# Kernel optimization log

Hardware: AMD Instinct MI355X
Metric: run time of the kernel (lower is better)

The kernel has to match this reference:

```python
import jax, jax.numpy as jnp
import numpy as np

N_FEATURE = 1024
N_HEAD = 16
DK = N_FEATURE // N_HEAD
SCALE = float(np.sqrt(DK))
LN_EPS = 1e-5


def setup_inputs() -> dict:
    key = jax.random.key(0)
    ks = jax.random.split(key, 12)
    B, T, F = 4, 2048, N_FEATURE
    s = 1.0 / np.sqrt(F)
    inp = {
        "key": jax.random.normal(ks[0], (B, T, F), jnp.float32),
        "value": jax.random.normal(ks[1], (B, T, F), jnp.float32),
        "query": jax.random.normal(ks[2], (B, T, F), jnp.float32),
        "Wq": jax.random.uniform(ks[3], (F, F), jnp.float32, -s, s),
        "bq": jax.random.uniform(ks[4], (F,), jnp.float32, -s, s),
        "Wk": jax.random.uniform(ks[5], (F, F), jnp.float32, -s, s),
        "bk": jax.random.uniform(ks[6], (F,), jnp.float32, -s, s),
        "Wv": jax.random.uniform(ks[7], (F, F), jnp.float32, -s, s),
        "bv": jax.random.uniform(ks[8], (F,), jnp.float32, -s, s),
        "Wo": jax.random.uniform(ks[9], (F, F), jnp.float32, -s, s),
        "bo": jax.random.uniform(ks[10], (F,), jnp.float32, -s, s),
        "ln_g": jnp.ones((F,), jnp.float32),
        "ln_b": jnp.zeros((F,), jnp.float32),
    }
    return inp


def reference(key, value, query, Wq, bq, Wk, bk, Wv, bv, Wo, bo, ln_g, ln_b):
    # key/value/query: [B, T, F]. torch chunk(n_head, -1) == reshape to (B,T,H,dk).
    B, T, F = query.shape
    residual = query
    q = (query @ Wq.T + bq).reshape(B, T, N_HEAD, DK)
    k = (key @ Wk.T + bk).reshape(B, T, N_HEAD, DK)
    v = (value @ Wv.T + bv).reshape(B, T, N_HEAD, DK)
    # scores: [B, H, Tq, Tk]
    scores = jnp.einsum("bqhd,bkhd->bhqk", q, k) / SCALE
    attn = jax.nn.softmax(scores, axis=-1)
    ctx = jnp.einsum("bhqk,bkhd->bqhd", attn, v).reshape(B, T, F)
    out = ctx @ Wo.T + bo  # dropout in eval mode = identity
    x = residual + out
    mu = jnp.mean(x, axis=-1, keepdims=True)
    var = jnp.mean(jnp.square(x - mu), axis=-1, keepdims=True)
    return (x - mu) * jax.lax.rsqrt(var + LN_EPS) * ln_g + ln_b
```

## Files before the change

### kernel.cpp

```cpp
#include <hip/hip_runtime.h>
#include <hip/hip_bf16.h>
#include <cstdint>
#include <cstddef>

#define DEVI __device__ __forceinline__

typedef __attribute__((ext_vector_type(8))) short short8;
typedef __attribute__((ext_vector_type(4))) float f32x4;
typedef __attribute__((ext_vector_type(16))) float f32x16;
typedef __attribute__((ext_vector_type(4))) unsigned int u32x4;

constexpr int Bz = 4, Tt = 2048, Fd = 1024, Hh = 16, Dk = 64;
constexpr int Mrows = Bz * Tt;
constexpr float QSCALE = 0.18033688011112042f;

DEVI unsigned short f2bf(float f) {
  union { __hip_bfloat16 h; unsigned short u; } cv;
  cv.h = __float2bfloat16(f);
  return cv.u;
}

DEVI unsigned cvtpk(float a, float b) {
  unsigned r;
  asm("v_cvt_pk_bf16_f32 %0, %1, %2" : "=v"(r) : "v"(a), "v"(b));
  return r;
}

DEVI void gl_lds16(const void* g, void* s) {
  __builtin_amdgcn_global_load_lds(
      (const __attribute__((address_space(1))) void*)g,
      (__attribute__((address_space(3))) void*)s, 16, 0, 0);
}

__global__ void cvt4_bf16(const float* __restrict__ s0, unsigned short* __restrict__ d0,
                          const float* __restrict__ s1, unsigned short* __restrict__ d1,
                          const float* __restrict__ s2, unsigned short* __restrict__ d2,
                          const float* __restrict__ s3, unsigned short* __restrict__ d3,
                          int n4) {
  const float* src = blockIdx.y == 0 ? s0 : (blockIdx.y == 1 ? s1 : (blockIdx.y == 2 ? s2 : s3));
  unsigned short* dst = blockIdx.y == 0 ? d0 : (blockIdx.y == 1 ? d1 : (blockIdx.y == 2 ? d2 : d3));
  int i = blockIdx.x * blockDim.x + threadIdx.x;
  int stride = gridDim.x * blockDim.x;
  for (; i < n4; i += stride) {
    float4 v = reinterpret_cast<const float4*>(src)[i];
    ushort4 o;
    o.x = f2bf(v.x); o.y = f2bf(v.y); o.z = f2bf(v.z); o.w = f2bf(v.w);
    reinterpret_cast<ushort4*>(dst)[i] = o;
  }
}

__global__ __launch_bounds__(256, 2) void gemm_qkvf(
    const float* __restrict__ q32, const float* __restrict__ k32,
    const float* __restrict__ v32, const unsigned short* __restrict__ wq,
    const unsigned short* __restrict__ wk, const unsigned short* __restrict__ wv,
    const float* __restrict__ bq, const float* __restrict__ bk, const float* __restrict__ bv,
    unsigned short* __restrict__ Qb, unsigned short* __restrict__ Kb,
    unsigned short* __restrict__ Vt) {
  constexpr int K = 1024, N = 1024;
  __shared__ __align__(16) unsigned short As[128 * 64];
  __shared__ __align__(16) unsigned short Bs[128 * 64];
  int z = blockIdx.z;
  const float* A32 = z == 0 ? q32 : (z == 1 ? k32 : v32);
  const unsigned short* W = z == 0 ? wq : (z == 1 ? wk : wv);
  const float* bias = z == 0 ? bq : (z == 1 ? bk : bv);
  void* out = z == 0 ? (void*)Qb : (z == 1 ? (void*)Kb : (void*)Vt);
  float scale = z == 0 ? QSCALE : 1.0f;
  int mode = z == 2 ? 2 : 0;

  int f = blockIdx.y * gridDim.x + blockIdx.x;
  f = (f & 7) * 64 + (f >> 3);
  const int m0 = (f >> 3) * 128, n0 = (f & 7) * 128;
  const int t = threadIdx.x, w = t >> 6, l = t & 63;
  const int wr = w >> 1, wc = w & 1;
  const int lr = l & 15, lg = l >> 4;
  f32x4 acc[4][4] = {};

  for (int k0 = 0; k0 < K; k0 += 64) {
    __syncthreads();
    float4 fA[4][2];
#pragma unroll
    for (int i = 0; i < 4; ++i) {
      int row = i * 32 + w * 8 + (l >> 3);
      const float* src = A32 + (size_t)(m0 + row) * K + k0 + (l & 7) * 8;
      fA[i][0] = ((const float4*)src)[0];
      fA[i][1] = ((const float4*)src)[1];
    }
#pragma unroll
    for (int i = 0; i < 4; ++i) {
      int base = i * 4096 + w * 1024;
      int d = base + l * 16;
      int row = d >> 7;
      int srcb = ((l & 7) ^ (row & 7)) << 4;
      gl_lds16((const char*)W + ((size_t)(n0 + row) * K + k0) * 2 + srcb, (char*)Bs + base);
    }
#pragma unroll
    for (int i = 0; i < 4; ++i) {
      int row = i * 32 + w * 8 + (l >> 3);
      u32x4 wv4;
      wv4[0] = cvtpk(fA[i][0].x, fA[i][0].y);
      wv4[1] = cvtpk(fA[i][0].z, fA[i][0].w);
      wv4[2] = cvtpk(fA[i][1].x, fA[i][1].y);
      wv4[3] = cvtpk(fA[i][1].z, fA[i][1].w);
      int slot = (l & 7) ^ (row & 7);
      *(u32x4*)((char*)As + row * 128 + slot * 16) = wv4;
    }
    __syncthreads();
#pragma unroll
    for (int kk = 0; kk < 2; ++kk) {
      short8 af[4], bf[4];
#pragma unroll
      for (int i = 0; i < 4; ++i) {
        int ra = wr * 64 + i * 16 + lr;
        int rb = wc * 64 + i * 16 + lr;
        af[i] = *(const short8*)((const char*)As + ra * 128 + (((kk * 4 + lg) ^ (ra & 7)) << 4));
        bf[i] = *(const short8*)((const char*)Bs + rb * 128 + (((kk * 4 + lg) ^ (rb & 7)) << 4));
      }
#pragma unroll
      for (int mi = 0; mi < 4; ++mi)
#pragma unroll
        for (int ni = 0; ni < 4; ++ni)
          acc[mi][ni] = __builtin_amdgcn_mfma_f32_16x16x32_bf16(af[mi], bf[ni], acc[mi][ni], 0, 0, 0);
    }
  }
#pragma unroll
  for (int mi = 0; mi < 4; ++mi)
#pragma unroll
    for (int ni = 0; ni < 4; ++ni) {
      int col = n0 + wc * 64 + ni * 16 + lr;
      float bv = bias[col];
      if (mode == 2) {
        int hh = col >> 6, dd = col & 63;
        int row = m0 + wr * 64 + mi * 16 + lg * 4;
        int bb = row >> 11, t0 = row & 2047;
        ushort4 o;
        o.x = f2bf(acc[mi][ni][0] + bv);
        o.y = f2bf(acc[mi][ni][1] + bv);
        o.z = f2bf(acc[mi][ni][2] + bv);
        o.w = f2bf(acc[mi][ni][3] + bv);
        *(ushort4*)((unsigned short*)out + (((size_t)(bb * Hh + hh) * Dk + dd) << 11) + t0) = o;
      } else {
#pragma unroll
        for (int r = 0; r < 4; ++r) {
          int row = m0 + wr * 64 + mi * 16 + lg * 4 + r;
          ((unsigned short*)out)[(size_t)row * N + col] = f2bf((acc[mi][ni][r] + bv) * scale);
        }
      }
    }
}

__global__ __launch_bounds__(256, 2) void gemm_out(
    const unsigned short* __restrict__ A, const unsigned short* __restrict__ W,
    const float* __restrict__ bias, const float* __restrict__ resid,
    float* __restrict__ out) {
  constexpr int K = 1024, N = 1024;
  __shared__ __align__(16) unsigned short As[128 * 64];
  __shared__ __align__(16) unsigned short Bs[128 * 64];
  int f = blockIdx.y * gridDim.x + blockIdx.x;
  f = (f & 7) * 64 + (f >> 3);
  const int m0 = (f >> 3) * 128, n0 = (f & 7) * 128;
  const int t = threadIdx.x, w = t >> 6, l = t & 63;
  const int wr = w >> 1, wc = w & 1;
  const int lr = l & 15, lg = l >> 4;
  f32x4 acc[4][4] = {};
  for (int k0 = 0; k0 < K; k0 += 64) {
    __syncthreads();
#pragma unroll
    for (int i = 0; i < 4; ++i) {
      int base = i * 4096 + w * 1024;
      int d = base + l * 16;
      int row = d >> 7;
      int srcb = ((l & 7) ^ (row & 7)) << 4;
      gl_lds16((const char*)A + ((size_t)(m0 + row) * K + k0) * 2 + srcb, (char*)As + base);
      gl_lds16((const char*)W + ((size_t)(n0 + row) * K + k0) * 2 + srcb, (char*)Bs + base);
    }
    __syncthreads();
#pragma unroll
    for (int kk = 0; kk < 2; ++kk) {
      short8 af[4], bf[4];
#pragma unroll
      for (int i = 0; i < 4; ++i) {
        int ra = wr * 64 + i * 16 + lr;
        int rb = wc * 64 + i * 16 + lr;
        af[i] = *(const short8*)((const char*)As + ra * 128 + (((kk * 4 + lg) ^ (ra & 7)) << 4));
        bf[i] = *(const short8*)((const char*)Bs + rb * 128 + (((kk * 4 + lg) ^ (rb & 7)) << 4));
      }
#pragma unroll
      for (int mi = 0; mi < 4; ++mi)
#pragma unroll
        for (int ni = 0; ni < 4; ++ni)
          acc[mi][ni] = __builtin_amdgcn_mfma_f32_16x16x32_bf16(af[mi], bf[ni], acc[mi][ni], 0, 0, 0);
    }
  }
#pragma unroll
  for (int mi = 0; mi < 4; ++mi)
#pragma unroll
    for (int ni = 0; ni < 4; ++ni) {
      int col = n0 + wc * 64 + ni * 16 + lr;
      float bv = bias[col];
#pragma unroll
      for (int r = 0; r < 4; ++r) {
        int row = m0 + wr * 64 + mi * 16 + lg * 4 + r;
        size_t idx = (size_t)row * N + col;
        out[idx] = acc[mi][ni][r] + bv + resid[idx];
      }
    }
}

__global__ __launch_bounds__(512, 2) void attn_kernel(
    const unsigned short* __restrict__ Qb, const unsigned short* __restrict__ Kb,
    const unsigned short* __restrict__ Vt, unsigned short* __restrict__ Ctx) {
  __shared__ __align__(16) unsigned short smem[16 * 4096];
  int bid = blockIdx.x;
  const int xcd = bid & 7, idx = bid >> 3;
  const int bh = xcd * 8 + (idx >> 2);
  const int q0 = (idx & 3) * 512;
  const int h = bh & 15;
  const int b = bh >> 4;
  const int t = threadIdx.x, w = t >> 6, l = t & 63;
  const int q31 = l & 31, hi = l >> 5;
  const int qbase = q0 + w * 64;

  short8 qfA[4], qfB[4];
  {
    const unsigned short* qpA = Qb + (size_t)(b * Tt + qbase + q31) * Fd + h * Dk;
    const unsigned short* qpB = qpA + (size_t)32 * Fd;
#pragma unroll
    for (int c = 0; c < 4; ++c) {
      qfA[c] = *(const short8*)(qpA + c * 16 + hi * 8);
      qfB[c] = *(const short8*)(qpB + c * 16 + hi * 8);
    }
  }

  int koff[8];
#pragma unroll
  for (int g = 0; g < 2; ++g)
#pragma unroll
    for (int c = 0; c < 4; ++c) {
      int row = g * 32 + q31;
      koff[g * 4 + c] = row * 128 + ((c * 32 + hi * 16) ^ ((row & 7) << 4));
    }

  const size_t kbase = (size_t)(b * Tt) * Fd + h * Dk;
  const size_t vbase = (size_t)((b * Hh + h) * Dk) * Tt;

  f32x16 OA0{}, OA1{}, OB0{}, OB1{};
  short8 pfA[4], pfB[4];
  float lsA0 = 0.f, lsB0 = 0.f, lsA1 = 0.f, lsB1 = 0.f;

  auto kbuf = [&](int kt) { return (const char*)smem + ((kt & 7) << 13); };
  auto vbuf = [&](int kt) { return (const char*)smem + 65536 + ((kt & 7) << 13); };

  auto stage = [&](int kt) {
    char* Kd = (char*)smem + ((kt & 7) << 13);
    char* Vd = (char*)smem + 65536 + ((kt & 7) << 13);
    int base = w * 1024;
    int d0 = base + l * 16;
    int row = d0 >> 7, inb = d0 & 127;
    int srcb = inb ^ ((row & 7) << 4);
    gl_lds16((const char*)Kb + (kbase + (size_t)(kt * 64 + row) * Fd) * 2 + srcb, Kd + base);
    gl_lds16((const char*)Vt + (vbase + (size_t)row * Tt + kt * 64) * 2 + srcb, Vd + base);
  };

  auto qk = [&](int kt, f32x16& S0a, f32x16& S1a, f32x16& S0b, f32x16& S1b) {
    const char* Kd = kbuf(kt);
    __builtin_amdgcn_s_setprio(1);
#pragma unroll
    for (int c = 0; c < 4; ++c) {
      short8 k0 = *(const short8*)(Kd + koff[c]);
      short8 k1 = *(const short8*)(Kd + koff[4 + c]);
      S0a = __builtin_amdgcn_mfma_f32_32x32x16_bf16(k0, qfA[c], S0a, 0, 0, 0);
      S1a = __builtin_amdgcn_mfma_f32_32x32x16_bf16(k1, qfA[c], S1a, 0, 0, 0);
      S0b = __builtin_amdgcn_mfma_f32_32x32x16_bf16(k0, qfB[c], S0b, 0, 0, 0);
      S1b = __builtin_amdgcn_mfma_f32_32x32x16_bf16(k1, qfB[c], S1b, 0, 0, 0);
    }
    __builtin_amdgcn_s_setprio(0);
  };

  auto pv = [&](int kt) {
    const char* Vd = vbuf(kt);
    __builtin_amdgcn_s_setprio(1);
#pragma unroll
    for (int db = 0; db < 2; ++db)
#pragma unroll
      for (int kvc = 0; kvc < 4; ++kvc) {
        short8 vf = *(const short8*)(Vd + koff[db * 4 + kvc]);
        if (db == 0) {
          OA0 = __builtin_amdgcn_mfma_f32_32x32x16_bf16(vf, pfA[kvc], OA0, 0, 0, 0);
          OB0 = __builtin_amdgcn_mfma_f32_32x32x16_bf16(vf, pfB[kvc], OB0, 0, 0, 0);
        } else {
          OA1 = __builtin_amdgcn_mfma_f32_32x32x16_bf16(vf, pfA[kvc], OA1, 0, 0, 0);
          OB1 = __builtin_amdgcn_mfma_f32_32x32x16_bf16(vf, pfB[kvc], OB1, 0, 0, 0);
        }
      }
    __builtin_amdgcn_s_setprio(0);
  };

  auto softmax_pack = [&](const f32x16& S0, const f32x16& S1, float& lsA, float& lsB, short8* pf) {
    unsigned pk0[8], pk1[8];
#pragma unroll
    for (int j = 0; j < 8; ++j) {
      int r = j * 2;
      float a0 = __builtin_amdgcn_exp2f(S0[r]);
      float a1 = __builtin_amdgcn_exp2f(S0[r + 1]);
      float b0 = __builtin_amdgcn_exp2f(S1[r]);
      float b1 = __builtin_amdgcn_exp2f(S1[r + 1]);
      lsA += a0 + a1;
      lsB += b0 + b1;
      pk0[j] = cvtpk(a0, a1);
      pk1[j] = cvtpk(b0, b1);
    }
#pragma unroll
    for (int kc = 0; kc < 2; ++kc) {
      unsigned a0 = pk0[kc * 4 + 0], a2 = pk0[kc * 4 + 2];
      unsigned a1 = pk0[kc * 4 + 1], a3 = pk0[kc * 4 + 3];
      asm("v_permlane32_swap_b32 %0, %1" : "+v"(a0), "+v"(a2));
      asm("v_permlane32_swap_b32 %0, %1" : "+v"(a1), "+v"(a3));
      unsigned b0 = pk1[kc * 4 + 0], b2 = pk1[kc * 4 + 2];
      unsigned b1 = pk1[kc * 4 + 1], b3 = pk1[kc * 4 + 3];
      asm("v_permlane32_swap_b32 %0, %1" : "+v"(b0), "+v"(b2));
      asm("v_permlane32_swap_b32 %0, %1" : "+v"(b1), "+v"(b3));
      u32x4 fa, fb;
      fa[0] = a0; fa[1] = a1; fa[2] = a2; fa[3] = a3;
      fb[0] = b0; fb[1] = b1; fb[2] = b2; fb[3] = b3;
      pf[kc] = __builtin_bit_cast(short8, fa);
      pf[2 + kc] = __builtin_bit_cast(short8, fb);
    }
  };

  stage(0); stage(1); stage(2); stage(3);
  asm volatile("s_waitcnt vmcnt(4)" ::: "memory");
  __builtin_amdgcn_s_barrier();
  stage(4); stage(5);
  {
    f32x16 S0a{}, S1a{}, S0b{}, S1b{};
    qk(0, S0a, S1a, S0b, S1b);
    softmax_pack(S0a, S1a, lsA0, lsB0, pfA);
    softmax_pack(S0b, S1b, lsA1, lsB1, pfB);
  }
  {
    f32x16 S0a{}, S1a{}, S0b{}, S1b{};
    qk(1, S0a, S1a, S0b, S1b);
    pv(0);
    softmax_pack(S0a, S1a, lsA0, lsB0, pfA);
    softmax_pack(S0b, S1b, lsA1, lsB1, pfB);
  }
  for (int p = 1; p < 15; ++p) {
    asm volatile("s_waitcnt vmcnt(4)" ::: "memory");
    __builtin_amdgcn_s_barrier();
    if (p < 14) { stage(2 * p + 4); stage(2 * p + 5); }
    {
      f32x16 S0a{}, S1a{}, S0b{}, S1b{};
      qk(2 * p, S0a, S1a, S0b, S1b);
      pv(2 * p - 1);
      softmax_pack(S0a, S1a, lsA0, lsB0, pfA);
      softmax_pack(S0b, S1b, lsA1, lsB1, pfB);
    }
    {
      f32x16 S0a{}, S1a{}, S0b{}, S1b{};
      qk(2 * p + 1, S0a, S1a, S0b, S1b);
      pv(2 * p);
      softmax_pack(S0a, S1a, lsA0, lsB0, pfA);
      softmax_pack(S0b, S1b, lsA1, lsB1, pfB);
    }
  }
  asm volatile("s_waitcnt vmcnt(0)" ::: "memory");
  __builtin_amdgcn_s_barrier();
  {
    f32x16 S0a{}, S1a{}, S0b{}, S1b{};
    qk(30, S0a, S1a, S0b, S1b);
    pv(29);
    softmax_pack(S0a, S1a, lsA0, lsB0, pfA);
    softmax_pack(S0b, S1b, lsA1, lsB1, pfB);
  }
  {
    f32x16 S0a{}, S1a{}, S0b{}, S1b{};
    qk(31, S0a, S1a, S0b, S1b);
    pv(30);
    softmax_pack(S0a, S1a, lsA0, lsB0, pfA);
    softmax_pack(S0b, S1b, lsA1, lsB1, pfB);
  }
  pv(31);
  __builtin_amdgcn_s_barrier();

  float ls0 = lsA0 + lsB0;
  ls0 += __shfl_xor(ls0, 32);
  float linv0 = 1.0f / ls0;
  float ls1 = lsA1 + lsB1;
  ls1 += __shfl_xor(ls1, 32);
  float linv1 = 1.0f / ls1;
  unsigned short* Ow = smem + w * 4096;
#pragma unroll
  for (int g = 0; g < 2; ++g) {
    float linv = g == 0 ? linv0 : linv1;
    int rowq = g * 32 + q31;
#pragma unroll
    for (int db = 0; db < 2; ++db)
#pragma unroll
      for (int rp = 0; rp < 8; ++rp) {
        int r = rp * 2;
        float a, b2;
        if (g == 0) {
          a = (db == 0 ? OA0[r] : OA1[r]) * linv;
          b2 = (db == 0 ? OA0[r + 1] : OA1[r + 1]) * linv;
        } else {
          a = (db == 0 ? OB0[r] : OB1[r]) * linv;
          b2 = (db == 0 ? OB0[r + 1] : OB1[r + 1]) * linv;
        }
        unsigned wv = cvtpk(a, b2);
        int dd = db * 32 + (r & 3) + 8 * (r >> 2) + 4 * hi;
        int byteo = (rowq * 128 + (dd >> 1) * 4) ^ ((rowq & 7) << 4);
        *(unsigned*)((char*)Ow + byteo) = wv;
      }
  }
#pragma unroll
  for (int i = 0; i < 8; ++i) {
    int qq = i * 8 + (l >> 3), slot = l & 7;
    int byteo = (qq * 128 + slot * 16) ^ ((qq & 7) << 4);
    short8 ov = *(const short8*)((const char*)Ow + byteo);
    *(short8*)(Ctx + (size_t)(b * Tt + qbase + qq) * Fd + h * Dk + slot * 8) = ov;
  }
}

__global__ __launch_bounds__(256) void ln_res(
    float* __restrict__ xo, const float* __restrict__ gamma, const float* __restrict__ beta) {
  int row = blockIdx.x, t = threadIdx.x;
  float4 xv = ((const float4*)(xo + (size_t)row * Fd))[t];
  float x0 = xv.x, x1 = xv.y, x2 = xv.z, x3 = xv.w;
  float s = x0 + x1 + x2 + x3;
  float ss = x0 * x0 + x1 * x1 + x2 * x2 + x3 * x3;
#pragma unroll
  for (int off = 32; off >= 1; off >>= 1) {
    s += __shfl_xor(s, off);
    ss += __shfl_xor(ss, off);
  }
  __shared__ float rs_[4], rss[4];
  int w = t >> 6, l = t & 63;
  if (l == 0) { rs_[w] = s; rss[w] = ss; }
  __syncthreads();
  s = rs_[0] + rs_[1] + rs_[2] + rs_[3];
  ss = rss[0] + rss[1] + rss[2] + rss[3];
  float mu = s * (1.0f / 1024.0f);
  float var = ss * (1.0f / 1024.0f) - mu * mu;
  float rstd = rsqrtf(var + 1e-5f);
  float4 gv = ((const float4*)gamma)[t];
  float4 bv = ((const float4*)beta)[t];
  float4 o;
  o.x = (x0 - mu) * rstd * gv.x + bv.x;
  o.y = (x1 - mu) * rstd * gv.y + bv.y;
  o.z = (x2 - mu) * rstd * gv.z + bv.z;
  o.w = (x3 - mu) * rstd * gv.w + bv.w;
  ((float4*)(xo + (size_t)row * Fd))[t] = o;
}

extern "C" void kernel_launch(void* const* d_in, const int* in_sizes, int n_in,
                              void* d_out, int out_size, void* d_ws, size_t ws_size,
                              hipStream_t stream) {
  (void)in_sizes; (void)n_in; (void)out_size; (void)ws_size;
  const float* key   = (const float*)d_in[0];
  const float* value = (const float*)d_in[1];
  const float* query = (const float*)d_in[2];
  const float* Wq = (const float*)d_in[3];
  const float* bq = (const float*)d_in[4];
  const float* Wk = (const float*)d_in[5];
  const float* bk = (const float*)d_in[6];
  const float* Wv = (const float*)d_in[7];
  const float* bv_ = (const float*)d_in[8];
  const float* Wo = (const float*)d_in[9];
  const float* bo = (const float*)d_in[10];
  const float* ln_g = (const float*)d_in[11];
  const float* ln_b = (const float*)d_in[12];
  float* out = (float*)d_out;

  char* ws = (char*)d_ws;
  size_t off = 0;
  auto alloc = [&](size_t bytes) {
    char* p = ws + off;
    off += (bytes + 255) & ~(size_t)255;
    return p;
  };
  const size_t MF = (size_t)Mrows * Fd;
  unsigned short* Qb  = (unsigned short*)alloc(MF * 2);
  unsigned short* Kbf = (unsigned short*)alloc(MF * 2);
  unsigned short* Vtb = (unsigned short*)alloc(MF * 2);
  unsigned short* Ctx = (unsigned short*)alloc(MF * 2);
  unsigned short* wqb = (unsigned short*)alloc((size_t)Fd * Fd * 2);
  unsigned short* wkb = (unsigned short*)alloc((size_t)Fd * Fd * 2);
  unsigned short* wvb = (unsigned short*)alloc((size_t)Fd * Fd * 2);
  unsigned short* wob = (unsigned short*)alloc((size_t)Fd * Fd * 2);

  cvt4_bf16<<<dim3(256, 4), 256, 0, stream>>>(Wq, wqb, Wk, wkb, Wv, wvb, Wo, wob, (Fd * Fd) / 4);

  gemm_qkvf<<<dim3(Fd / 128, Mrows / 128, 3), 256, 0, stream>>>(
      query, key, value, wqb, wkb, wvb, bq, bk, bv_, Qb, Kbf, Vtb);

  attn_kernel<<<Bz * Hh * (Tt / 512), 512, 0, stream>>>(Qb, Kbf, Vtb, Ctx);

  gemm_out<<<dim3(Fd / 128, Mrows / 128), 256, 0, stream>>>(Ctx, wob, bo, query, out);
  ln_res<<<Mrows, 256, 0, stream>>>(out, ln_g, ln_b);
}
```

Before: 180.9 us.

## Fuse LayerNorm into output GEMM using cooperative grid sync

Folds the residual-add and LayerNorm into the output projection GEMM. Each block computes per-row partial sums and sums of squares for its 128-column slice, writes them to global scratch, then synchronises the whole grid cooperatively before reading all eight partials to normalise from registers. This removes the separate LN kernel launch and the extra fp32 write/read round trip of the output. In exchange the grid must be co-resident (512 blocks at two per CU), and the grid-wide barrier stalls early-finishing blocks.

Measured after the change: 296.7 us. 1.64x slower.

```diff
diff --git a/kernel.cpp b/kernel.cpp
--- a/kernel.cpp
+++ b/kernel.cpp
@@ -1,7 +1,10 @@
 #include <hip/hip_runtime.h>
 #include <hip/hip_bf16.h>
+#include <hip/hip_cooperative_groups.h>
 #include <cstdint>
 #include <cstddef>
+
+namespace cg = cooperative_groups;
 
 #define DEVI __device__ __forceinline__
 
@@ -148,9 +151,11 @@
     }
 }
 
-__global__ __launch_bounds__(256, 2) void gemm_out(
+__global__ __launch_bounds__(256, 2) void gemm_out_ln(
     const unsigned short* __restrict__ A, const unsigned short* __restrict__ W,
     const float* __restrict__ bias, const float* __restrict__ resid,
+    const float* __restrict__ gamma, const float* __restrict__ beta,
+    float* __restrict__ psum, float* __restrict__ pssq,
     float* __restrict__ out) {
   constexpr int K = 1024, N = 1024;
   __shared__ __align__(16) unsigned short As[128 * 64];
@@ -158,6 +163,7 @@
   int f = blockIdx.y * gridDim.x + blockIdx.x;
   f = (f & 7) * 64 + (f >> 3);
   const int m0 = (f >> 3) * 128, n0 = (f & 7) * 128;
+  const int nblk = n0 >> 7;
   const int t = threadIdx.x, w = t >> 6, l = t & 63;
   const int wr = w >> 1, wc = w & 1;
   const int lr = l & 15, lg = l >> 4;
@@ -191,17 +197,81 @@
           acc[mi][ni] = __builtin_amdgcn_mfma_f32_16x16x32_bf16(af[mi], bf[ni], acc[mi][ni], 0, 0, 0);
     }
   }
+
+  __syncthreads();
+  float* lsum = (float*)As;
+  float* lssq = lsum + 256;
+  float* lmu  = lssq + 256;
+  float* lrs  = lmu + 128;
+
+  float gv[4], bvv[4], biasv[4];
+#pragma unroll
+  for (int ni = 0; ni < 4; ++ni) {
+    int col = n0 + wc * 64 + ni * 16 + lr;
+    biasv[ni] = bias[col];
+    gv[ni] = gamma[col];
+    bvv[ni] = beta[col];
+  }
+#pragma unroll
+  for (int mi = 0; mi < 4; ++mi) {
+#pragma unroll
+    for (int r = 0; r < 4; ++r) {
+      int row = m0 + wr * 64 + mi * 16 + lg * 4 + r;
+      float s = 0.f, q = 0.f;
+#pragma unroll
+      for (int ni = 0; ni < 4; ++ni) {
+        int col = n0 + wc * 64 + ni * 16 + lr;
+        float x = acc[mi][ni][r] + biasv[ni] + resid[(size_t)row * N + col];
+        acc[mi][ni][r] = x;
+        s += x;
+        q += x * x;
+      }
+#pragma unroll
+      for (int off = 1; off <= 8; off <<= 1) {
+        s += __shfl_xor(s, off);
+        q += __shfl_xor(q, off);
+      }
+      if (lr == 0) {
+        int rowl = wr * 64 + mi * 16 + lg * 4 + r;
+        lsum[wc * 128 + rowl] = s;
+        lssq[wc * 128 + rowl] = q;
+      }
+    }
+  }
+  __syncthreads();
+  if (t < 128) {
+    float s = lsum[t] + lsum[128 + t];
+    float q = lssq[t] + lssq[128 + t];
+    psum[(size_t)(m0 + t) * 8 + nblk] = s;
+    pssq[(size_t)(m0 + t) * 8 + nblk] = q;
+  }
+  __threadfence();
+  cg::this_grid().sync();
+
+  if (t < 128) {
+    float s = 0.f, q = 0.f;
+#pragma unroll
+    for (int j = 0; j < 8; ++j) {
+      s += psum[(size_t)(m0 + t) * 8 + j];
+      q += pssq[(size_t)(m0 + t) * 8 + j];
+    }
+    float mu = s * (1.0f / 1024.0f);
+    float var = q * (1.0f / 1024.0f) - mu * mu;
+    lmu[t] = mu;
+    lrs[t] = rsqrtf(var + 1e-5f);
+  }
+  __syncthreads();
 #pragma unroll
   for (int mi = 0; mi < 4; ++mi)
 #pragma unroll
-    for (int ni = 0; ni < 4; ++ni) {
-      int col = n0 + wc * 64 + ni * 16 + lr;
-      float bv = bias[col];
-#pragma unroll
-      for (int r = 0; r < 4; ++r) {
-        int row = m0 + wr * 64 + mi * 16 + lg * 4 + r;
-        size_t idx = (size_t)row * N + col;
-        out[idx] = acc[mi][ni][r] + bv + resid[idx];
+    for (int r = 0; r < 4; ++r) {
+      int rowl = wr * 64 + mi * 16 + lg * 4 + r;
+      float mu = lmu[rowl], rs = lrs[rowl];
+      int row = m0 + rowl;
+#pragma unroll
+      for (int ni = 0; ni < 4; ++ni) {
+        int col = n0 + wc * 64 + ni * 16 + lr;
+        out[(size_t)row * N + col] = (acc[mi][ni][r] - mu) * rs * gv[ni] + bvv[ni];
       }
     }
 }
@@ -419,37 +489,6 @@
     short8 ov = *(const short8*)((const char*)Ow + byteo);
     *(short8*)(Ctx + (size_t)(b * Tt + qbase + qq) * Fd + h * Dk + slot * 8) = ov;
   }
-}
-
-__global__ __launch_bounds__(256) void ln_res(
-    float* __restrict__ xo, const float* __restrict__ gamma, const float* __restrict__ beta) {
-  int row = blockIdx.x, t = threadIdx.x;
-  float4 xv = ((const float4*)(xo + (size_t)row * Fd))[t];
-  float x0 = xv.x, x1 = xv.y, x2 = xv.z, x3 = xv.w;
-  float s = x0 + x1 + x2 + x3;
-  float ss = x0 * x0 + x1 * x1 + x2 * x2 + x3 * x3;
-#pragma unroll
-  for (int off = 32; off >= 1; off >>= 1) {
-    s += __shfl_xor(s, off);
-    ss += __shfl_xor(ss, off);
-  }
-  __shared__ float rs_[4], rss[4];
-  int w = t >> 6, l = t & 63;
-  if (l == 0) { rs_[w] = s; rss[w] = ss; }
-  __syncthreads();
-  s = rs_[0] + rs_[1] + rs_[2] + rs_[3];
-  ss = rss[0] + rss[1] + rss[2] + rss[3];
-  float mu = s * (1.0f / 1024.0f);
-  float var = ss * (1.0f / 1024.0f) - mu * mu;
-  float rstd = rsqrtf(var + 1e-5f);
-  float4 gv = ((const float4*)gamma)[t];
-  float4 bv = ((const float4*)beta)[t];
-  float4 o;
-  o.x = (x0 - mu) * rstd * gv.x + bv.x;
-  o.y = (x1 - mu) * rstd * gv.y + bv.y;
-  o.z = (x2 - mu) * rstd * gv.z + bv.z;
-  o.w = (x3 - mu) * rstd * gv.w + bv.w;
-  ((float4*)(xo + (size_t)row * Fd))[t] = o;
 }
 
 extern "C" void kernel_launch(void* const* d_in, const int* in_sizes, int n_in,
@@ -487,6 +526,8 @@
   unsigned short* wkb = (unsigned short*)alloc((size_t)Fd * Fd * 2);
   unsigned short* wvb = (unsigned short*)alloc((size_t)Fd * Fd * 2);
   unsigned short* wob = (unsigned short*)alloc((size_t)Fd * Fd * 2);
+  float* psum = (float*)alloc((size_t)Mrows * 8 * 4);
+  float* pssq = (float*)alloc((size_t)Mrows * 8 * 4);
 
   cvt4_bf16<<<dim3(256, 4), 256, 0, stream>>>(Wq, wqb, Wk, wkb, Wv, wvb, Wo, wob, (Fd * Fd) / 4);
 
@@ -495,6 +536,12 @@
 
   attn_kernel<<<Bz * Hh * (Tt / 512), 512, 0, stream>>>(Qb, Kbf, Vtb, Ctx);
 
-  gemm_out<<<dim3(Fd / 128, Mrows / 128), 256, 0, stream>>>(Ctx, wob, bo, query, out);
-  ln_res<<<Mrows, 256, 0, stream>>>(out, ln_g, ln_b);
-}
+  {
+    const unsigned short* A = Ctx;
+    const unsigned short* W = wob;
+    void* args[] = {(void*)&A, (void*)&W, (void*)&bo, (void*)&query,
+                    (void*)&ln_g, (void*)&ln_b, (void*)&psum, (void*)&pssq, (void*)&out};
+    hipLaunchCooperativeKernel((void*)gemm_out_ln, dim3(Fd / 128, Mrows / 128),
+                               dim3(256), args, 0, stream);
+  }
+}
```
